# Performance work log

Hardware: AMD Instinct MI355X
Metric: run time of the kernel (lower is better)

## Reference

```python
import jax, jax.numpy as jnp
from jax import lax
import numpy as np

KSIZE = 3
NUM_GAB = 16
NUM_IMAP = 16
BATCH = 4096


def gabor_bank(theta, sigma, gamma, lambd, psi, ksize=KSIZE):
    # vectorized version of the original triple Python loop
    offs = jnp.arange(ksize, dtype=theta.dtype) - 1.0  # (x-1), (y-1) in source
    xg, yg = jnp.meshgrid(offs, offs, indexing='ij')   # [K,K]
    c = jnp.cos(theta)[:, None, None]
    s = jnp.sin(theta)[:, None, None]
    xt = xg * c + yg * s        # [F,K,K]
    yt = -xg * s + yg * c
    sx = sigma[:, None, None]
    sy = (sigma / gamma)[:, None, None]
    env = jnp.exp(-0.5 * (xt ** 2 / sx ** 2 + yt ** 2 / sy ** 2))
    car = jnp.cos(2.0 * jnp.pi * xt / lambd[:, None, None] + psi[:, None, None])
    return env * car  # [F,K,K]


def maxpool2(x):
    return lax.reduce_window(x, -jnp.inf, lax.max, (1, 1, 2, 2), (1, 1, 2, 2), 'VALID')


def setup_inputs() -> dict:
    key = jax.random.key(0)
    ks = jax.random.split(key, 12)
    x = jax.random.normal(ks[0], (BATCH, 1, 28, 28), dtype=jnp.float32)
    theta = jax.random.uniform(ks[1], (NUM_GAB,), minval=0.0, maxval=180.0)
    sigma = jax.random.uniform(ks[2], (NUM_GAB,), minval=0.0, maxval=360.0)
    gamma = jax.random.uniform(ks[3], (NUM_GAB,), minval=0.0, maxval=1.0)
    lambd = jax.random.uniform(ks[4], (NUM_GAB,), minval=2.0, maxval=10.0)
    psi = jnp.zeros((NUM_GAB,), dtype=jnp.float32)
    conv2_w = jax.random.normal(ks[5], (64, 32, 3, 3), dtype=jnp.float32) * 0.05
    conv2_b = jnp.zeros((64,), dtype=jnp.float32)
    fc1_w = jax.random.normal(ks[6], (128, 3136), dtype=jnp.float32) * 0.02
    fc1_b = jnp.zeros((128,), dtype=jnp.float32)
    fc2_w = jax.random.normal(ks[7], (10, 128), dtype=jnp.float32) * 0.1
    fc2_b = jnp.zeros((10,), dtype=jnp.float32)
    return dict(x=x, theta=theta, sigma=sigma, gamma=gamma, lambd=lambd, psi=psi,
                conv2_w=conv2_w, conv2_b=conv2_b, fc1_w=fc1_w, fc1_b=fc1_b,
                fc2_w=fc2_w, fc2_b=fc2_b)


def reference(x, theta, sigma, gamma, lambd, psi, conv2_w, conv2_b, fc1_w, fc1_b, fc2_w, fc2_b):
    kern = gabor_bank(theta, sigma, gamma, lambd, psi)          # [16,3,3]
    imaps = jnp.zeros((NUM_IMAP, KSIZE, KSIZE), dtype=x.dtype).at[:, 1, 1].set(1.0)
    w1 = jnp.concatenate([kern, imaps], axis=0)[:, None]         # [32,1,3,3]
    dn = ('NCHW', 'OIHW', 'NCHW')
    out = lax.conv_general_dilated(x, w1, (1, 1), [(1, 1), (1, 1)], dimension_numbers=dn)
    out = maxpool2(jax.nn.relu(out))                             # [B,32,14,14]
    out = lax.conv_general_dilated(out, conv2_w, (1, 1), [(1, 1), (1, 1)], dimension_numbers=dn)
    out = maxpool2(jax.nn.relu(out + conv2_b[None, :, None, None]))  # [B,64,7,7]
    out = out.reshape(out.shape[0], -1)                          # [B,3136]
    out = jax.nn.relu(out @ fc1_w.T + fc1_b)                     # dropout = identity (eval)
    out = out @ fc2_w.T + fc2_b                                  # [B,10]
    return out
```

## Files before the change

kernel.cpp:

```cpp
#include <hip/hip_runtime.h>
#include <hip/hip_bf16.h>

#define BATCH 4096

typedef unsigned short u16;
typedef _Float16 half2v __attribute__((ext_vector_type(2)));
typedef _Float16 half4 __attribute__((ext_vector_type(4)));
typedef _Float16 half8 __attribute__((ext_vector_type(8)));
typedef short bs8 __attribute__((ext_vector_type(8)));
typedef u16 u16x4 __attribute__((ext_vector_type(4)));
typedef float floatx4 __attribute__((ext_vector_type(4)));
typedef float floatx16 __attribute__((ext_vector_type(16)));

__device__ inline u16 f2bf_hw(float f) {
    __hip_bfloat16 b = __float2bfloat16(f);
    return *(u16*)&b;
}

__global__ __launch_bounds__(256) void prep_kernel(
        const float* __restrict__ theta, const float* __restrict__ sigma,
        const float* __restrict__ gamma, const float* __restrict__ lambd,
        const float* __restrict__ psi, const float* __restrict__ conv2_w,
        const float* __restrict__ fc1_w, _Float16* __restrict__ w1h,
        _Float16* __restrict__ w2h, u16* __restrict__ wbf) {
    int id = blockIdx.x * 256 + threadIdx.x;
    if (id < 512) {
        int g = id >> 4, t = id & 15;
        float v = 0.0f;
        if (t < 9) {
            int i = t / 3, j = t % 3;
            float xg = (float)i - 1.0f;
            float yg = (float)j - 1.0f;
            if (g < 16) {
                float th = theta[g];
                float c = cosf(th), s = sinf(th);
                float xt = xg * c + yg * s;
                float yt = -xg * s + yg * c;
                float sx = sigma[g];
                float sy = sx / gamma[g];
                float env = expf(-0.5f *
                                 (xt * xt / (sx * sx) + yt * yt / (sy * sy)));
                float car =
                    cosf(6.28318530717958647692f * xt / lambd[g] + psi[g]);
                v = env * car;
            } else {
                v = (t == 4) ? 1.0f : 0.0f;
            }
        }
        w1h[id] = (_Float16)v;
    } else if (id < 512 + 18432) {
        int t2 = id - 512;
        int tap = t2 / 2048, rem = t2 % 2048;
        int oc = rem / 32, k = rem % 32;
        int ic = (k >> 1) + 16 * (k & 1);
        w2h[t2] = (_Float16)conv2_w[(oc * 32 + ic) * 9 + tap];
    } else {
        int i4 = id - 18944;
        int s = i4 >> 10;
        int q = i4 & 1023;
        int row = q >> 3;
        int kp = s * 32 + (q & 7) * 4;
        int pl = kp >> 6;
        int ocb = kp & 63;
        const float* src = fc1_w + row * 3136 + ocb * 49 + pl;
        u16x4 o;
        o[0] = f2bf_hw(src[0]);
        o[1] = f2bf_hw(src[49]);
        o[2] = f2bf_hw(src[98]);
        o[3] = f2bf_hw(src[147]);
        ((u16x4*)wbf)[(size_t)s * 1024 + row * 8 + (q & 7)] = o;
    }
}

__global__ __launch_bounds__(256, 4) void fused_conv_kernel(
        const float* __restrict__ x, const _Float16* __restrict__ w1h,
        const _Float16* __restrict__ w2h, const float* __restrict__ conv2_b,
        u16* __restrict__ a2) {
    __shared__ _Float16 img16[30][36];
    __shared__ __align__(16) _Float16 a1s[16][16][40];
    __shared__ __align__(16) u16 out2[64 * 49];

    int t = threadIdx.x;
    int n0 = blockIdx.x * 2;
    int lane = t & 63;
    int w = t >> 6;
    int l16 = lane & 15;
    int quad = lane >> 4;
    int l32 = lane & 31;
    int h = lane >> 5;

    int nt = w & 1;
    int mt0 = w >> 1;
    int oc = nt * 32 + l32;

    half4 b1a = *(const half4*)&w1h[l16 * 16 + quad * 4];
    half4 b1b = *(const half4*)&w1h[(16 + l16) * 16 + quad * 4];
    int t0 = quad * 4;
    int u0 = t0 < 9 ? t0 : 8, u1 = t0 + 1 < 9 ? t0 + 1 : 8;
    int u2 = t0 + 2 < 9 ? t0 + 2 : 8, u3 = t0 + 3 < 9 ? t0 + 3 : 8;
    int off0 = (u0 / 3) * 36 + (u0 % 3);
    int off1 = (u1 / 3) * 36 + (u1 % 3);
    int off2 = (u2 / 3) * 36 + (u2 % 3);
    int off3 = (u3 / 3) * 36 + (u3 % 3);
    int sy = (l16 & 3) >> 1, sx = l16 & 1;

    int pool0 = w * 4 + (l16 >> 2);
    int a14_s = pool0 >= 14 ? 1 : 0;
    int b14_s = pool0 - 14 * a14_s;
    int pl0 = w * 4 + quad;
    int pa_s = pl0 >= 14 ? 1 : 0;
    int pb_s = pl0 - 14 * pa_s;

    auto conv1_body = [&]() {
        int a14 = a14_s, b14 = b14_s, pa = pa_s, pb = pb_s;
        for (int mt = w; mt < 49; mt += 4) {
            const _Float16* p = &img16[2 * a14 + sy][2 * b14 + sx];
            half4 av;
            av[0] = p[off0];
            av[1] = p[off1];
            av[2] = p[off2];
            av[3] = p[off3];
            floatx4 c0 = {0.f, 0.f, 0.f, 0.f};
            floatx4 c1 = {0.f, 0.f, 0.f, 0.f};
            c0 = __builtin_amdgcn_mfma_f32_16x16x16f16(av, b1a, c0, 0, 0, 0);
            c1 = __builtin_amdgcn_mfma_f32_16x16x16f16(av, b1b, c1, 0, 0, 0);
            float m0 = fmaxf(fmaxf(c0[0], c0[1]), fmaxf(c0[2], c0[3]));
            float m1 = fmaxf(fmaxf(c1[0], c1[1]), fmaxf(c1[2], c1[3]));
            half2v pk;
            pk[0] = (_Float16)fmaxf(m0, 0.0f);
            pk[1] = (_Float16)fmaxf(m1, 0.0f);
            *(half2v*)&a1s[1 + pa][1 + pb][2 * l16] = pk;
            a14 += 1; b14 += 2;
            if (b14 >= 14) { b14 -= 14; a14 += 1; }
            pa += 1; pb += 2;
            if (pb >= 14) { pb -= 14; pa += 1; }
        }
    };

    if (t < 240) {
        int pos = t >> 2, ch = t & 3;
        int r, c;
        if (pos < 16)      { r = 0;        c = pos; }
        else if (pos < 32) { r = 15;       c = pos - 16; }
        else if (pos < 46) { r = pos - 31; c = 0; }
        else               { r = pos - 45; c = 15; }
        *(int4*)&a1s[r][c][ch * 8] = int4{0, 0, 0, 0};
    }
    const float* xim0 = x + (size_t)n0 * 784;
    for (int i = t; i < 960; i += 256) {
        int r = i >> 5, c = i & 31;
        bool inter = (r >= 1) & (r <= 28) & (c >= 1) & (c <= 28);
        float v = inter ? xim0[(r - 1) * 28 + (c - 1)] : 0.0f;
        img16[r][c] = (_Float16)v;
    }
    __syncthreads();

    const float* xim1 = x + (size_t)(n0 + 1) * 784;
    float gx[4];
#pragma unroll
    for (int j = 0; j < 4; ++j) {
        int i = t + j * 256;
        gx[j] = (i < 784) ? xim1[i] : 0.0f;
    }
    conv1_body();
    half8 bE[9], bO[9];
    {
        const _Float16* bp = w2h + (size_t)oc * 32 + h * 8;
#pragma unroll
        for (int tt = 0; tt < 9; ++tt) {
            bE[tt] = *(const half8*)(bp + tt * 2048);
            bO[tt] = *(const half8*)(bp + tt * 2048 + 16);
        }
    }
    float bias = conv2_b[oc];
    __syncthreads();

    auto conv2_body = [&]() {
        for (int mt = mt0; mt < 7; mt += 2) {
            int pool = mt * 8 + (l32 >> 2);
            int sub = l32 & 3;
            int pc = pool < 49 ? pool : 48;
            int y = 2 * (pc / 7) + (sub >> 1);
            int xq = 2 * (pc % 7) + (sub & 1);
            const _Float16* ap = &a1s[y][xq][h * 8];
            floatx16 acc = {};
#pragma unroll
            for (int tt = 0; tt < 9; ++tt) {
                int ao = ((tt / 3) * 16 + (tt % 3)) * 40;
                half8 avE = *(const half8*)(ap + ao);
                half8 avO = *(const half8*)(ap + ao + 16);
                acc = __builtin_amdgcn_mfma_f32_32x32x16_f16(avE, bE[tt], acc,
                                                             0, 0, 0);
                acc = __builtin_amdgcn_mfma_f32_32x32x16_f16(avO, bO[tt], acc,
                                                             0, 0, 0);
            }
#pragma unroll
            for (int rg = 0; rg < 4; ++rg) {
                int pl = mt * 8 + 2 * rg + h;
                if (pl < 49) {
                    float v0 = acc[rg * 4 + 0];
                    float v1 = acc[rg * 4 + 1];
                    float v2 = acc[rg * 4 + 2];
                    float v3 = acc[rg * 4 + 3];
                    float mx = fmaxf(fmaxf(v0, v1), fmaxf(v2, v3));
                    out2[pl * 64 + oc] = f2bf_hw(fmaxf(mx + bias, 0.0f));
                }
            }
        }
    };

    auto copyout = [&](int n) {
        uint2* dst = (uint2*)a2;
        const uint2* src = (const uint2*)&out2[0];
        size_t n8 = (size_t)n * 8;
        for (int i = t; i < 784; i += 256) {
            int s = i >> 3, off = i & 7;
            dst[(size_t)s * 32768 + n8 + off] = src[i];
        }
    };

#pragma unroll
    for (int j = 0; j < 4; ++j) {
        int i = t + j * 256;
        if (i < 784) img16[i / 28 + 1][i % 28 + 1] = (_Float16)gx[j];
    }
    conv2_body();
    __syncthreads();

    copyout(n0);
    conv1_body();
    __syncthreads();

    conv2_body();
    __syncthreads();

    copyout(n0 + 1);
}

__global__ __launch_bounds__(1024) void fc_kernel(
        const u16* __restrict__ A, const u16* __restrict__ Wbf,
        const float* __restrict__ fc1_b, const float* __restrict__ fc2_w,
        const float* __restrict__ fc2_b, float* __restrict__ out) {
    __shared__ float Hs[8][16][132];
    int tid = threadIdx.x;
    int lane = tid & 63;
    int w = tid >> 6;
    int l16 = lane & 15;
    int quad = lane >> 4;
    int kq = w >> 1;
    int nh = w & 1;
    int m0 = blockIdx.x * 16;

    const u16* abase = A + (size_t)(m0 + l16) * 32 + quad * 8;
    const u16* bbase = Wbf + (size_t)(nh * 64 + l16) * 32 + quad * 8;

    floatx4 ac0 = {0.f, 0.f, 0.f, 0.f};
    floatx4 ac1 = {0.f, 0.f, 0.f, 0.f};
    floatx4 ac2 = {0.f, 0.f, 0.f, 0.f};
    floatx4 ac3 = {0.f, 0.f, 0.f, 0.f};
#pragma unroll 4
    for (int s = kq; s < 98; s += 8) {
        bs8 av = *(const bs8*)(abase + (size_t)s * 131072);
        const u16* bt = bbase + (size_t)s * 4096;
        bs8 bv0 = *(const bs8*)(bt);
        bs8 bv1 = *(const bs8*)(bt + 512);
        bs8 bv2 = *(const bs8*)(bt + 1024);
        bs8 bv3 = *(const bs8*)(bt + 1536);
        ac0 = __builtin_amdgcn_mfma_f32_16x16x32_bf16(av, bv0, ac0, 0, 0, 0);
        ac1 = __builtin_amdgcn_mfma_f32_16x16x32_bf16(av, bv1, ac1, 0, 0, 0);
        ac2 = __builtin_amdgcn_mfma_f32_16x16x32_bf16(av, bv2, ac2, 0, 0, 0);
        ac3 = __builtin_amdgcn_mfma_f32_16x16x32_bf16(av, bv3, ac3, 0, 0, 0);
    }
    int nb = nh * 64 + l16;
#pragma unroll
    for (int r = 0; r < 4; ++r) {
        int mr = quad * 4 + r;
        Hs[kq][mr][nb] = ac0[r];
        Hs[kq][mr][nb + 16] = ac1[r];
        Hs[kq][mr][nb + 32] = ac2[r];
        Hs[kq][mr][nb + 48] = ac3[r];
    }
    __syncthreads();

    for (int i = tid; i < 2048; i += 1024) {
        int m = i >> 7, k = i & 127;
        float s = Hs[0][m][k] + Hs[1][m][k] + Hs[2][m][k] + Hs[3][m][k] +
                  Hs[4][m][k] + Hs[5][m][k] + Hs[6][m][k] + Hs[7][m][k];
        Hs[0][m][k] = s;
    }
    __syncthreads();

    if (tid < 160) {
        int m = tid / 10, j = tid % 10;
        const float* wr = fc2_w + j * 128;
        float acc = fc2_b[j];
#pragma unroll 16
        for (int k = 0; k < 128; ++k)
            acc += fmaxf(Hs[0][m][k] + fc1_b[k], 0.0f) * wr[k];
        out[(size_t)(m0 + m) * 10 + j] = acc;
    }
}

extern "C" void kernel_launch(void* const* d_in, const int* in_sizes, int n_in,
                              void* d_out, int out_size, void* d_ws,
                              size_t ws_size, hipStream_t stream) {
    const float* x       = (const float*)d_in[0];
    const float* theta   = (const float*)d_in[1];
    const float* sigma   = (const float*)d_in[2];
    const float* gamma   = (const float*)d_in[3];
    const float* lambd   = (const float*)d_in[4];
    const float* psi     = (const float*)d_in[5];
    const float* conv2_w = (const float*)d_in[6];
    const float* conv2_b = (const float*)d_in[7];
    const float* fc1_w   = (const float*)d_in[8];
    const float* fc1_b   = (const float*)d_in[9];
    const float* fc2_w   = (const float*)d_in[10];
    const float* fc2_b   = (const float*)d_in[11];
    float* out = (float*)d_out;

    char* ws = (char*)d_ws;
    u16* a2 = (u16*)ws;
    _Float16* w1h = (_Float16*)(ws + 25690112ull);
    _Float16* w2h = (_Float16*)(ws + 25691136ull);
    u16* wbf = (u16*)(ws + 25728000ull);

    prep_kernel<<<466, 256, 0, stream>>>(theta, sigma, gamma, lambd, psi,
                                         conv2_w, fc1_w, w1h, w2h, wbf);
    fused_conv_kernel<<<BATCH / 2, 256, 0, stream>>>(x, w1h, w2h, conv2_b,
                                                     a2);
    fc_kernel<<<BATCH / 16, 1024, 0, stream>>>(a2, wbf, fc1_b, fc2_w, fc2_b,
                                               out);
}
```

Before: 147.2 us.

## Write conv2 outputs directly to global, split MFMA accumulators, pad a1s rows

Removes the out2 shared staging buffer and its copyout loop, so conv2 results go straight to global memory as 2-byte stores, which drops one barrier per image. The MFMA chain is split into two independent accumulators (even and odd K halves) to shorten the dependency chain. The a1s row stride is padded from 16 to 17 to reduce LDS bank conflicts. The trade-off is that the global stores become scattered 16-bit writes instead of coalesced 8-byte copies, and the extra accumulator raises register pressure.

```diff
diff --git a/kernel.cpp b/kernel.cpp
--- a/kernel.cpp
+++ b/kernel.cpp
@@ -77,8 +77,7 @@
         const _Float16* __restrict__ w2h, const float* __restrict__ conv2_b,
         u16* __restrict__ a2) {
     __shared__ _Float16 img16[30][36];
-    __shared__ __align__(16) _Float16 a1s[16][16][40];
-    __shared__ __align__(16) u16 out2[64 * 49];
+    __shared__ __align__(16) _Float16 a1s[16][17][40];
 
     int t = threadIdx.x;
     int n0 = blockIdx.x * 2;
@@ -175,7 +174,7 @@
     float bias = conv2_b[oc];
     __syncthreads();
 
-    auto conv2_body = [&]() {
+    auto conv2_body = [&](int n) {
         for (int mt = mt0; mt < 7; mt += 2) {
             int pool = mt * 8 + (l32 >> 2);
             int sub = l32 & 3;
@@ -183,58 +182,46 @@
             int y = 2 * (pc / 7) + (sub >> 1);
             int xq = 2 * (pc % 7) + (sub & 1);
             const _Float16* ap = &a1s[y][xq][h * 8];
-            floatx16 acc = {};
+            floatx16 accE = {};
+            floatx16 accO = {};
 #pragma unroll
             for (int tt = 0; tt < 9; ++tt) {
-                int ao = ((tt / 3) * 16 + (tt % 3)) * 40;
+                int ao = (tt / 3) * (17 * 40) + (tt % 3) * 40;
                 half8 avE = *(const half8*)(ap + ao);
                 half8 avO = *(const half8*)(ap + ao + 16);
-                acc = __builtin_amdgcn_mfma_f32_32x32x16_f16(avE, bE[tt], acc,
-                                                             0, 0, 0);
-                acc = __builtin_amdgcn_mfma_f32_32x32x16_f16(avO, bO[tt], acc,
-                                                             0, 0, 0);
+                accE = __builtin_amdgcn_mfma_f32_32x32x16_f16(avE, bE[tt],
+                                                              accE, 0, 0, 0);
+                accO = __builtin_amdgcn_mfma_f32_32x32x16_f16(avO, bO[tt],
+                                                              accO, 0, 0, 0);
             }
 #pragma unroll
             for (int rg = 0; rg < 4; ++rg) {
                 int pl = mt * 8 + 2 * rg + h;
                 if (pl < 49) {
-                    float v0 = acc[rg * 4 + 0];
-                    float v1 = acc[rg * 4 + 1];
-                    float v2 = acc[rg * 4 + 2];
-                    float v3 = acc[rg * 4 + 3];
+                    float v0 = accE[rg * 4 + 0] + accO[rg * 4 + 0];
+                    float v1 = accE[rg * 4 + 1] + accO[rg * 4 + 1];
+                    float v2 = accE[rg * 4 + 2] + accO[rg * 4 + 2];
+                    float v3 = accE[rg * 4 + 3] + accO[rg * 4 + 3];
                     float mx = fmaxf(fmaxf(v0, v1), fmaxf(v2, v3));
-                    out2[pl * 64 + oc] = f2bf_hw(fmaxf(mx + bias, 0.0f));
+                    a2[((size_t)(pl * 2 + nt) * 4096 + n) * 32 + l32] =
+                        f2bf_hw(fmaxf(mx + bias, 0.0f));
                 }
             }
         }
     };
 
-    auto copyout = [&](int n) {
-        uint2* dst = (uint2*)a2;
-        const uint2* src = (const uint2*)&out2[0];
-        size_t n8 = (size_t)n * 8;
-        for (int i = t; i < 784; i += 256) {
-            int s = i >> 3, off = i & 7;
-            dst[(size_t)s * 32768 + n8 + off] = src[i];
-        }
-    };
-
 #pragma unroll
     for (int j = 0; j < 4; ++j) {
         int i = t + j * 256;
         if (i < 784) img16[i / 28 + 1][i % 28 + 1] = (_Float16)gx[j];
     }
-    conv2_body();
-    __syncthreads();
-
-    copyout(n0);
+    conv2_body(n0);
+    __syncthreads();
+
     conv1_body();
     __syncthreads();
 
-    conv2_body();
-    __syncthreads();
-
-    copyout(n0 + 1);
+    conv2_body(n0 + 1);
 }
 
 __global__ __launch_bounds__(1024) void fc_kernel(
```

Result: slower. 171.5 us (+16.5%).

## XOR-swizzle conv1 activation tile in LDS and split conv2 MFMA accumulators

Applied to the files above, without the earlier changes.

Applies an XOR swizzle on the column index of the padded conv1 activation tile in shared memory. The conv1 writes, border zeroing and conv2 reads all use the same swizzle, which is meant to reduce LDS bank conflicts on the half8 loads. The conv2 inner loop now uses two independent accumulators (even and odd channel halves) that are summed at the end, breaking the serial MFMA dependency chain. This costs extra accumulator registers and per-tap index arithmetic.

```diff
diff --git a/kernel.cpp b/kernel.cpp
--- a/kernel.cpp
+++ b/kernel.cpp
@@ -129,7 +129,9 @@
             half2v pk;
             pk[0] = (_Float16)fmaxf(m0, 0.0f);
             pk[1] = (_Float16)fmaxf(m1, 0.0f);
-            *(half2v*)&a1s[1 + pa][1 + pb][2 * l16] = pk;
+            int row = 1 + pa;
+            int colp = (1 + pb) ^ (2 * (row & 3));
+            *(half2v*)&a1s[row][colp][2 * l16] = pk;
             a14 += 1; b14 += 2;
             if (b14 >= 14) { b14 -= 14; a14 += 1; }
             pa += 1; pb += 2;
@@ -144,7 +146,8 @@
         else if (pos < 32) { r = 15;       c = pos - 16; }
         else if (pos < 46) { r = pos - 31; c = 0; }
         else               { r = pos - 45; c = 15; }
-        *(int4*)&a1s[r][c][ch * 8] = int4{0, 0, 0, 0};
+        int colp = c ^ (2 * (r & 3));
+        *(int4*)&a1s[r][colp][ch * 8] = int4{0, 0, 0, 0};
     }
     const float* xim0 = x + (size_t)n0 * 784;
     for (int i = t; i < 960; i += 256) {
@@ -182,26 +185,33 @@
             int pc = pool < 49 ? pool : 48;
             int y = 2 * (pc / 7) + (sub >> 1);
             int xq = 2 * (pc % 7) + (sub & 1);
-            const _Float16* ap = &a1s[y][xq][h * 8];
-            floatx16 acc = {};
-#pragma unroll
-            for (int tt = 0; tt < 9; ++tt) {
-                int ao = ((tt / 3) * 16 + (tt % 3)) * 40;
-                half8 avE = *(const half8*)(ap + ao);
-                half8 avO = *(const half8*)(ap + ao + 16);
-                acc = __builtin_amdgcn_mfma_f32_32x32x16_f16(avE, bE[tt], acc,
-                                                             0, 0, 0);
-                acc = __builtin_amdgcn_mfma_f32_32x32x16_f16(avO, bO[tt], acc,
-                                                             0, 0, 0);
+            floatx16 accE = {};
+            floatx16 accO = {};
+#pragma unroll
+            for (int dy = 0; dy < 3; ++dy) {
+                int row = y + dy;
+                int sw = 2 * (row & 3);
+                const _Float16* rp = &a1s[row][0][h * 8];
+#pragma unroll
+                for (int dx = 0; dx < 3; ++dx) {
+                    int tt = dy * 3 + dx;
+                    const _Float16* ap = rp + ((xq + dx) ^ sw) * 40;
+                    half8 avE = *(const half8*)(ap);
+                    half8 avO = *(const half8*)(ap + 16);
+                    accE = __builtin_amdgcn_mfma_f32_32x32x16_f16(
+                        avE, bE[tt], accE, 0, 0, 0);
+                    accO = __builtin_amdgcn_mfma_f32_32x32x16_f16(
+                        avO, bO[tt], accO, 0, 0, 0);
+                }
             }
 #pragma unroll
             for (int rg = 0; rg < 4; ++rg) {
                 int pl = mt * 8 + 2 * rg + h;
                 if (pl < 49) {
-                    float v0 = acc[rg * 4 + 0];
-                    float v1 = acc[rg * 4 + 1];
-                    float v2 = acc[rg * 4 + 2];
-                    float v3 = acc[rg * 4 + 3];
+                    float v0 = accE[rg * 4 + 0] + accO[rg * 4 + 0];
+                    float v1 = accE[rg * 4 + 1] + accO[rg * 4 + 1];
+                    float v2 = accE[rg * 4 + 2] + accO[rg * 4 + 2];
+                    float v3 = accE[rg * 4 + 3] + accO[rg * 4 + 3];
                     float mx = fmaxf(fmaxf(v0, v1), fmaxf(v2, v3));
                     out2[pl * 64 + oc] = f2bf_hw(fmaxf(mx + bias, 0.0f));
                 }
```

Result: slower. 159.5 us (+8.3%).
